# Optimization experiments

Measured on AMD Instinct MI355X. Metric: run time of the kernel, lower is better.

## Reference

```python
import jax, jax.numpy as jnp
import numpy as np

D_MODEL = 1024
NUM_HEADS = 16
DEPTH = D_MODEL // NUM_HEADS
B, S = 2, 2048
NEG = -1e9


def setup_inputs() -> dict:
    key = jax.random.key(0)
    ks = jax.random.split(key, 12)
    sc = 1.0 / np.sqrt(D_MODEL)
    inp = {
        "query": jax.random.normal(ks[0], (B, S, D_MODEL), jnp.float32),
        "key_in": jax.random.normal(ks[1], (B, S, D_MODEL), jnp.float32),
        "value": jax.random.normal(ks[2], (B, S, D_MODEL), jnp.float32),
        # causal mask: 1.0 where attention is disallowed (upper triangle)
        "mask": (1.0 - jnp.tril(jnp.ones((S, S), jnp.float32)))[None, None, :, :],
        "wq": jax.random.normal(ks[3], (D_MODEL, D_MODEL), jnp.float32) * sc,
        "bq": jnp.zeros((D_MODEL,), jnp.float32),
        "wk": jax.random.normal(ks[4], (D_MODEL, D_MODEL), jnp.float32) * sc,
        "bk": jnp.zeros((D_MODEL,), jnp.float32),
        "wv": jax.random.normal(ks[5], (D_MODEL, D_MODEL), jnp.float32) * sc,
        "bv": jnp.zeros((D_MODEL,), jnp.float32),
        "wo": jax.random.normal(ks[6], (D_MODEL, D_MODEL), jnp.float32) * sc,
        "bo": jnp.zeros((D_MODEL,), jnp.float32),
    }
    return inp


def _split_heads(x):
    # [B,S,D] -> [B,H,S,depth]
    b, s, _ = x.shape
    return x.reshape(b, s, NUM_HEADS, DEPTH).transpose(0, 2, 1, 3)


def reference(query, key_in, value, mask, wq, bq, wk, bk, wv, bv, wo, bo):
    q = _split_heads(query @ wq + bq)
    k = _split_heads(key_in @ wk + bk)
    v = _split_heads(value @ wv + bv)
    scale = 1.0 / jnp.sqrt(jnp.asarray(DEPTH, jnp.float32))
    logits = jnp.einsum("bhqd,bhkd->bhqk", q, k) * scale + mask * NEG
    attn = jax.nn.softmax(logits, axis=-1)
    out = jnp.einsum("bhqk,bhkd->bhqd", attn, v)  # [B,H,S,depth]
    out = out.transpose(0, 2, 1, 3).reshape(query.shape[0], -1, D_MODEL)
    return out @ wo + bo
```

## Files before the change

### kernel.cpp

```cpp
#include <hip/hip_runtime.h>
#include <hip/hip_bf16.h>
#include <cstdint>
#include <cstddef>

#define D_MODEL 1024
#define NHEADS  16
#define DEPTH   64
#define BATCH   2
#define SEQ     2048
#define M_TOT   (BATCH*SEQ)
#define QK_SCALE 0.18033688011112042f

typedef __attribute__((ext_vector_type(8)))  __bf16 bf16x8;
typedef __attribute__((ext_vector_type(4)))  float  f32x4;
typedef __attribute__((ext_vector_type(16))) float  f32x16;

__device__ inline unsigned short f2bf(float f){
  unsigned u = __float_as_uint(f);
  u += 0x7FFFu + ((u>>16)&1u);
  return (unsigned short)(u>>16);
}
__device__ inline unsigned cvtpk(float lo, float hi){
  unsigned r;
  asm("v_cvt_pk_bf16_f32 %0, %1, %2" : "=v"(r) : "v"(lo), "v"(hi));
  return r;
}
__device__ inline float fexp2(float x){
  float r;
  asm("v_exp_f32 %0, %1" : "=v"(r) : "v"(x));
  return r;
}
__device__ inline int bswap23(int x){
  return (x & ~12) | ((x & 4) << 1) | ((x & 8) >> 1);
}

#define AS1(p) ((__attribute__((address_space(1))) void*)(p))
#define AS3(p) ((__attribute__((address_space(3))) void*)(p))

__global__ void cvt3(const float* __restrict__ q, const float* __restrict__ k,
                     const float* __restrict__ v,
                     unsigned short* oq, unsigned short* ok, unsigned short* ov, int n4){
  const float* in = blockIdx.z==0 ? q : blockIdx.z==1 ? k : v;
  unsigned short* out = blockIdx.z==0 ? oq : blockIdx.z==1 ? ok : ov;
  int i = blockIdx.x*blockDim.x + threadIdx.x;
  if (i >= n4) return;
  float4 val = ((const float4*)in)[i];
  ushort4 o;
  o.x = f2bf(val.x); o.y = f2bf(val.y); o.z = f2bf(val.z); o.w = f2bf(val.w);
  ((ushort4*)out)[i] = o;
}

__global__ void tcvt4(const float* __restrict__ w0, const float* __restrict__ w1,
                      const float* __restrict__ w2, const float* __restrict__ w3,
                      unsigned short* o0, unsigned short* o1,
                      unsigned short* o2, unsigned short* o3){
  const float* W = blockIdx.z==0 ? w0 : blockIdx.z==1 ? w1 : blockIdx.z==2 ? w2 : w3;
  unsigned short* Wt = blockIdx.z==0 ? o0 : blockIdx.z==1 ? o1 : blockIdx.z==2 ? o2 : o3;
  const bool perm = (blockIdx.z == 3);
  __shared__ float t[32][33];
  int bx = blockIdx.x*32, by = blockIdx.y*32;
  for (int j = threadIdx.y; j < 32; j += 8)
    t[j][threadIdx.x] = W[(size_t)(by+j)*D_MODEL + bx + threadIdx.x];
  __syncthreads();
  for (int j = threadIdx.y; j < 32; j += 8){
    int col = by + threadIdx.x;
    if (perm) col = bswap23(col);
    Wt[(size_t)(bx+j)*D_MODEL + col] = f2bf(t[threadIdx.x][j]);
  }
}

#define BM 128
#define BN 128
#define BK 32
#define GK 1024

#define GEMM_BODY(As, Bs, Abase, Bbase, acc) \
  for (int k0 = 0; k0 < GK; k0 += BK){ \
    _Pragma("unroll") \
    for (int c=0;c<2;c++){ \
      __builtin_amdgcn_global_load_lds( \
        AS1(Abase + (size_t)(c*64 + (tid>>2))*(GK*2) + k0*2 + (tid&3)*16), \
        AS3((char*)As + c*4096 + tid*16), 16, 0, 0); \
      __builtin_amdgcn_global_load_lds( \
        AS1(Bbase + (size_t)(c*64 + (tid>>2))*(GK*2) + k0*2 + (tid&3)*16), \
        AS3((char*)Bs + c*4096 + tid*16), 16, 0, 0); \
    } \
    __syncthreads(); \
    bf16x8 af[4], bfv[4]; \
    _Pragma("unroll") \
    for (int i=0;i<4;i++) \
      af[i] = *(const bf16x8*)((const char*)As + (wm*64 + i*16 + (lane&15))*64 + (lane>>4)*16); \
    _Pragma("unroll") \
    for (int j=0;j<4;j++) \
      bfv[j] = *(const bf16x8*)((const char*)Bs + (wn*64 + j*16 + (lane&15))*64 + (lane>>4)*16); \
    _Pragma("unroll") \
    for (int i=0;i<4;i++) \
      _Pragma("unroll") \
      for (int j=0;j<4;j++) \
        acc[i][j] = __builtin_amdgcn_mfma_f32_16x16x32_bf16(af[i], bfv[j], acc[i][j], 0,0,0); \
    __syncthreads(); \
  }

__global__ __launch_bounds__(256,2) void gemm_qkv(
    const unsigned short* __restrict__ Xq, const unsigned short* __restrict__ Xk,
    const unsigned short* __restrict__ Xv,
    const unsigned short* __restrict__ Wq, const unsigned short* __restrict__ Wk,
    const unsigned short* __restrict__ Wv,
    const float* __restrict__ bq, const float* __restrict__ bk, const float* __restrict__ bv,
    unsigned short* Qh, unsigned short* Kh, unsigned short* Vth)
{
  __shared__ __align__(16) short As[BM*BK];
  __shared__ __align__(16) short Bs[BN*BK];
  const int z = blockIdx.z;
  const unsigned short* A  = z==0 ? Xq : z==1 ? Xk : Xv;
  const unsigned short* Bt = z==0 ? Wq : z==1 ? Wk : Wv;
  const float* bias        = z==0 ? bq : z==1 ? bk : bv;

  const int tid = threadIdx.x, lane = tid & 63, wave = tid >> 6;
  const int m0 = blockIdx.x*BM, n0 = blockIdx.y*BN;
  const int wm = wave >> 1, wn = wave & 1;

  f32x4 acc[4][4];
  #pragma unroll
  for (int i=0;i<4;i++)
    #pragma unroll
    for (int j=0;j<4;j++)
      acc[i][j] = (f32x4){0.f,0.f,0.f,0.f};

  const char* Abase = (const char*)A + (size_t)m0*GK*2;
  const char* Bbase = (const char*)Bt + (size_t)n0*GK*2;

  GEMM_BODY(As, Bs, Abase, Bbase, acc)

  #pragma unroll
  for (int i=0;i<4;i++)
    #pragma unroll
    for (int j=0;j<4;j++)
      #pragma unroll
      for (int r=0;r<4;r++){
        int gr = m0 + wm*64 + i*16 + (lane>>4)*4 + r;
        int gc = n0 + wn*64 + j*16 + (lane&15);
        float v = acc[i][j][r] + bias[gc];
        int b = gr>>11, s = gr&2047, h = gc>>6, d = gc&63;
        if (z == 0){
          v *= QK_SCALE;
          Qh[(((size_t)(b*NHEADS+h))*SEQ + s)*DEPTH + d] = f2bf(v);
        } else if (z == 1){
          Kh[(((size_t)(b*NHEADS+h))*SEQ + s)*DEPTH + d] = f2bf(v);
        } else {
          int sp = bswap23(s);
          Vth[(((size_t)(b*NHEADS+h))*DEPTH + d)*SEQ + sp] = f2bf(v);
        }
      }
}

#define BM2 64
__global__ __launch_bounds__(256,2) void gemm_out(
    const unsigned short* __restrict__ A,
    const unsigned short* __restrict__ Bt,
    const float* __restrict__ bias,
    float* __restrict__ Cout)
{
  __shared__ __align__(16) short As[BM2*BK];
  __shared__ __align__(16) short Bs[BN*BK];
  const int tid = threadIdx.x, lane = tid & 63, wave = tid >> 6;
  const int m0 = blockIdx.x*BM2, n0 = blockIdx.y*BN;
  const int wm = wave >> 1, wn = wave & 1;

  f32x4 acc[2][4];
  #pragma unroll
  for (int i=0;i<2;i++)
    #pragma unroll
    for (int j=0;j<4;j++)
      acc[i][j] = (f32x4){0.f,0.f,0.f,0.f};

  const char* Abase = (const char*)A + (size_t)m0*GK*2;
  const char* Bbase = (const char*)Bt + (size_t)n0*GK*2;

  for (int k0 = 0; k0 < GK; k0 += BK){
    __builtin_amdgcn_global_load_lds(
      AS1(Abase + (size_t)(tid>>2)*(GK*2) + k0*2 + (tid&3)*16),
      AS3((char*)As + tid*16), 16, 0, 0);
    #pragma unroll
    for (int c=0;c<2;c++)
      __builtin_amdgcn_global_load_lds(
        AS1(Bbase + (size_t)(c*64 + (tid>>2))*(GK*2) + k0*2 + (tid&3)*16),
        AS3((char*)Bs + c*4096 + tid*16), 16, 0, 0);
    __syncthreads();
    bf16x8 af[2], bfv[4];
    #pragma unroll
    for (int i=0;i<2;i++)
      af[i] = *(const bf16x8*)((const char*)As + (wm*32 + i*16 + (lane&15))*64 + (lane>>4)*16);
    #pragma unroll
    for (int j=0;j<4;j++)
      bfv[j] = *(const bf16x8*)((const char*)Bs + (wn*64 + j*16 + (lane&15))*64 + (lane>>4)*16);
    #pragma unroll
    for (int i=0;i<2;i++)
      #pragma unroll
      for (int j=0;j<4;j++)
        acc[i][j] = __builtin_amdgcn_mfma_f32_16x16x32_bf16(af[i], bfv[j], acc[i][j], 0,0,0);
    __syncthreads();
  }

  #pragma unroll
  for (int i=0;i<2;i++)
    #pragma unroll
    for (int j=0;j<4;j++)
      #pragma unroll
      for (int r=0;r<4;r++){
        int gr = m0 + wm*32 + i*16 + (lane>>4)*4 + r;
        int gc = n0 + wn*64 + j*16 + (lane&15);
        Cout[(size_t)gr*D_MODEL + gc] = acc[i][j][r] + bias[gc];
      }
}

__global__ __launch_bounds__(512,4) void attn_fwd(
  const unsigned short* __restrict__ Qh,
  const unsigned short* __restrict__ Kh,
  const unsigned short* __restrict__ Vt,
  unsigned short* __restrict__ AO)
{
  __shared__ __align__(16) short Ks[2][4096];
  __shared__ __align__(16) short Vs[2][4096];
  __shared__ float cbS[2][128];

  const int tid = threadIdx.x, lane = tid & 63, w = tid >> 6;
  const int h = lane >> 5, ql = lane & 31;
  const int qh = w & 1, kh = (w >> 1) & 1, tl = w >> 2;
  const int pj = blockIdx.x, bh = blockIdx.y;
  const size_t hb = (size_t)bh * SEQ * DEPTH;
  const char* Kb = (const char*)(Kh + hb);
  const char* Vb = (const char*)(Vt + hb);
  const unsigned short* Qb = Qh + hb;
  const int bb = bh >> 4, hd = bh & 15;
  const int swz = (ql & 7) << 4;

  auto STAGE = [&](int buf, int t){
    const int kv0 = t*64;
    #pragma unroll
    for (int i=0;i<2;i++){
      int c = (w&3)*2 + i;
      int x = c*1024 + lane*16;
      int row = x >> 7;
      int cb = (x & 127) ^ ((row&7)<<4);
      if (w < 4)
        __builtin_amdgcn_global_load_lds(
          AS1(Kb + (size_t)(kv0+row)*128 + cb),
          AS3((char*)&Ks[buf][0] + c*1024), 16, 0, 0);
      else
        __builtin_amdgcn_global_load_lds(
          AS1(Vb + ((size_t)row*SEQ + kv0)*2 + cb),
          AS3((char*)&Vs[buf][0] + c*1024), 16, 0, 0);
    }
  };

  const int jtw = tl ? pj : (31 - pj);
  const int Q0 = jtw*64 + qh*32;
  const int qmax = Q0 + 31;
  const int Tblock = 32 - pj;

  bf16x8 qreg[4];
  {
    const unsigned short* qp = Qb + (size_t)(Q0 + ql)*DEPTH + h*8;
    #pragma unroll
    for (int c=0;c<4;c++) qreg[c] = *(const bf16x8*)(qp + c*16);
  }

  f32x16 oacc[2];
  #pragma unroll
  for (int dh=0;dh<2;dh++)
    #pragma unroll
    for (int r=0;r<16;r++) oacc[dh][r] = 0.f;
  float s = 0.f;

  STAGE(0, 0);
  __syncthreads();
  int cur = 0;

  #pragma unroll 1
  for (int t = 0; t < Tblock; ++t){
    if (t+1 < Tblock) STAGE(cur^1, t+1);
    const int kvb = t*64 + kh*32;

    if (kvb <= qmax){
      f32x16 sa;
      #pragma unroll
      for (int r=0;r<16;r++) sa[r] = -16.0f;
      #pragma unroll
      for (int c=0;c<4;c++){
        bf16x8 kf = *(const bf16x8*)((const char*)&Ks[cur][0]
                      + (kh*32 + ql)*128 + ((32*c + 16*h) ^ swz));
        sa = __builtin_amdgcn_mfma_f32_32x32x16_bf16(kf, qreg[c], sa, 0,0,0);
      }

      if (kvb + 31 > Q0){
        const int qg = Q0 + ql - kvb;
        #pragma unroll
        for (int r=0;r<16;r++){
          int pos = (r&3) + 8*(r>>2) + 4*h;
          sa[r] = (pos > qg) ? -1e9f : sa[r];
        }
      }

      float s0=0.f, s1=0.f, s2=0.f, s3=0.f;
      #pragma unroll
      for (int r=0;r<16;r++){
        float p = fexp2(sa[r]);
        sa[r] = p;
        if ((r&3)==0) s0 += p; else if ((r&3)==1) s1 += p;
        else if ((r&3)==2) s2 += p; else s3 += p;
      }
      s += (s0+s1)+(s2+s3);

      bf16x8 pw[2];
      #pragma unroll
      for (int ks=0;ks<2;ks++){
        const int mm = 8*ks;
        union { unsigned u[4]; bf16x8 v; } pk;
        pk.u[0] = cvtpk(sa[mm+0], sa[mm+1]);
        pk.u[1] = cvtpk(sa[mm+2], sa[mm+3]);
        pk.u[2] = cvtpk(sa[mm+4], sa[mm+5]);
        pk.u[3] = cvtpk(sa[mm+6], sa[mm+7]);
        pw[ks] = pk.v;
      }

      #pragma unroll
      for (int ks=0;ks<2;ks++){
        #pragma unroll
        for (int dh=0;dh<2;dh++){
          bf16x8 vf = *(const bf16x8*)((const char*)&Vs[cur][0]
                        + (dh*32 + ql)*128 + ((kh*64 + ks*32 + 16*h) ^ swz));
          oacc[dh] = __builtin_amdgcn_mfma_f32_32x32x16_bf16(vf, pw[ks], oacc[dh], 0,0,0);
        }
      }
    }

    __syncthreads();
    cur ^= 1;
  }

  float* cbO  = (tl == 0) ? (float*)&Ks[0][0] : (float*)&Vs[0][0];
  float* cbSp = &cbS[tl][0];
  if (kh == 1){
    #pragma unroll
    for (int dh=0;dh<2;dh++)
      #pragma unroll
      for (int r=0;r<16;r++)
        cbO[(dh*16+r)*128 + qh*64 + lane] = oacc[dh][r];
    cbSp[qh*64 + lane] = s;
  }
  __syncthreads();
  if (kh == 0){
    #pragma unroll
    for (int dh=0;dh<2;dh++)
      #pragma unroll
      for (int r=0;r<16;r++)
        oacc[dh][r] += cbO[(dh*16+r)*128 + qh*64 + lane];
    s += cbSp[qh*64 + lane];
    float st = s + __shfl_xor(s, 32, 64);
    float inv = 1.0f / st;
    #pragma unroll
    for (int dh=0;dh<2;dh++)
      #pragma unroll
      for (int r=0;r<16;r++) oacc[dh][r] *= inv;

    unsigned short* orow = AO + ((size_t)bb*SEQ + (Q0 + ql))*D_MODEL + hd*DEPTH;
    #pragma unroll
    for (int dh=0;dh<2;dh++)
      #pragma unroll
      for (int g=0; g<2; g++){
        uint4 st4;
        st4.x = cvtpk(oacc[dh][8*g+0], oacc[dh][8*g+1]);
        st4.y = cvtpk(oacc[dh][8*g+2], oacc[dh][8*g+3]);
        st4.z = cvtpk(oacc[dh][8*g+4], oacc[dh][8*g+5]);
        st4.w = cvtpk(oacc[dh][8*g+6], oacc[dh][8*g+7]);
        *(uint4*)(orow + dh*32 + g*16 + h*8) = st4;
      }
  }
}

extern "C" void kernel_launch(void* const* d_in, const int* in_sizes, int n_in,
                              void* d_out, int out_size, void* d_ws, size_t ws_size,
                              hipStream_t stream) {
  const float* query  = (const float*)d_in[0];
  const float* key_in = (const float*)d_in[1];
  const float* value  = (const float*)d_in[2];
  const float* wq = (const float*)d_in[4];
  const float* bq = (const float*)d_in[5];
  const float* wk = (const float*)d_in[6];
  const float* bk = (const float*)d_in[7];
  const float* wv = (const float*)d_in[8];
  const float* bv = (const float*)d_in[9];
  const float* wo = (const float*)d_in[10];
  const float* bo = (const float*)d_in[11];

  char* ws = (char*)d_ws;
  const size_t MB = 1u<<20;
  unsigned short* Xq  = (unsigned short*)(ws + 0*MB);
  unsigned short* Xk  = (unsigned short*)(ws + 8*MB);
  unsigned short* Xv  = (unsigned short*)(ws + 16*MB);
  unsigned short* Wtq = (unsigned short*)(ws + 24*MB);
  unsigned short* Wtk = (unsigned short*)(ws + 26*MB);
  unsigned short* Wtv = (unsigned short*)(ws + 28*MB);
  unsigned short* Wto = (unsigned short*)(ws + 30*MB);
  unsigned short* Qh  = (unsigned short*)(ws + 32*MB);
  unsigned short* Kh  = (unsigned short*)(ws + 40*MB);
  unsigned short* Vth = (unsigned short*)(ws + 48*MB);
  unsigned short* AO  = (unsigned short*)(ws + 56*MB);

  const int n4 = (M_TOT*D_MODEL)/4;
  cvt3<<<dim3(n4/256,1,3), 256, 0, stream>>>(query, key_in, value, Xq, Xk, Xv, n4);
  tcvt4<<<dim3(32,32,4), dim3(32,8), 0, stream>>>(wq, wk, wv, wo, Wtq, Wtk, Wtv, Wto);

  gemm_qkv<<<dim3(M_TOT/BM, D_MODEL/BN, 3), 256, 0, stream>>>(
      Xq, Xk, Xv, Wtq, Wtk, Wtv, bq, bk, bv, Qh, Kh, Vth);

  attn_fwd<<<dim3(16, BATCH*NHEADS), 512, 0, stream>>>(Qh, Kh, Vth, AO);

  gemm_out<<<dim3(M_TOT/BM2, D_MODEL/BN), 256, 0, stream>>>(AO, Wto, bo, (float*)d_out);
}
```

Measured before the change: 113.6 us.

## Double GEMM K-tile depth and XOR-swizzle LDS layout to cut bank conflicts

The QKV and output-projection GEMMs now stage a 64-wide K slice per iteration instead of 32, which halves the number of barrier pairs per K loop. The LDS rows become 128 bytes and are XOR-swizzled by row, applied both on the global_load_lds destination mapping and on the fragment reads, to avoid bank conflicts on the MFMA operand loads. The launch-bounds occupancy hint of 2 is removed. LDS use per block roughly doubles, which may reduce how many blocks fit on a CU.

```diff
diff --git a/kernel.cpp b/kernel.cpp
--- a/kernel.cpp
+++ b/kernel.cpp
@@ -71,37 +71,25 @@
 
 #define BM 128
 #define BN 128
-#define BK 32
+#define BK 64
 #define GK 1024
 
-#define GEMM_BODY(As, Bs, Abase, Bbase, acc) \
-  for (int k0 = 0; k0 < GK; k0 += BK){ \
-    _Pragma("unroll") \
-    for (int c=0;c<2;c++){ \
-      __builtin_amdgcn_global_load_lds( \
-        AS1(Abase + (size_t)(c*64 + (tid>>2))*(GK*2) + k0*2 + (tid&3)*16), \
-        AS3((char*)As + c*4096 + tid*16), 16, 0, 0); \
-      __builtin_amdgcn_global_load_lds( \
-        AS1(Bbase + (size_t)(c*64 + (tid>>2))*(GK*2) + k0*2 + (tid&3)*16), \
-        AS3((char*)Bs + c*4096 + tid*16), 16, 0, 0); \
-    } \
-    __syncthreads(); \
-    bf16x8 af[4], bfv[4]; \
-    _Pragma("unroll") \
-    for (int i=0;i<4;i++) \
-      af[i] = *(const bf16x8*)((const char*)As + (wm*64 + i*16 + (lane&15))*64 + (lane>>4)*16); \
-    _Pragma("unroll") \
-    for (int j=0;j<4;j++) \
-      bfv[j] = *(const bf16x8*)((const char*)Bs + (wn*64 + j*16 + (lane&15))*64 + (lane>>4)*16); \
-    _Pragma("unroll") \
-    for (int i=0;i<4;i++) \
-      _Pragma("unroll") \
-      for (int j=0;j<4;j++) \
-        acc[i][j] = __builtin_amdgcn_mfma_f32_16x16x32_bf16(af[i], bfv[j], acc[i][j], 0,0,0); \
-    __syncthreads(); \
-  }
-
-__global__ __launch_bounds__(256,2) void gemm_qkv(
+#define STAGE_TILE(lds, P, RSB, k0, ROWS) \
+  _Pragma("unroll") \
+  for (int i2=0; i2<(ROWS)/32; i2++){ \
+    int x = i2*4096 + tid*16; \
+    int row_ = x >> 7; \
+    int cb_ = (x & 127) ^ ((row_&7)<<4); \
+    __builtin_amdgcn_global_load_lds( \
+      AS1((P) + (size_t)row_*(RSB) + (k0)*2 + cb_), \
+      AS3((char*)(lds) + x), 16, 0, 0); \
+  }
+
+#define FRAG(lds, row_, kk) \
+  (*(const bf16x8*)((const char*)(lds) + (row_)*128 + \
+     (((kk)*64 + (lane>>4)*16) ^ (((row_)&7)<<4))))
+
+__global__ __launch_bounds__(256) void gemm_qkv(
     const unsigned short* __restrict__ Xq, const unsigned short* __restrict__ Xk,
     const unsigned short* __restrict__ Xv,
     const unsigned short* __restrict__ Wq, const unsigned short* __restrict__ Wk,
@@ -130,7 +118,27 @@
   const char* Abase = (const char*)A + (size_t)m0*GK*2;
   const char* Bbase = (const char*)Bt + (size_t)n0*GK*2;
 
-  GEMM_BODY(As, Bs, Abase, Bbase, acc)
+  for (int k0 = 0; k0 < GK; k0 += BK){
+    STAGE_TILE(As, Abase, GK*2, k0, BM)
+    STAGE_TILE(Bs, Bbase, GK*2, k0, BN)
+    __syncthreads();
+    #pragma unroll
+    for (int kk=0;kk<2;kk++){
+      bf16x8 af[4], bfv[4];
+      #pragma unroll
+      for (int i=0;i<4;i++)
+        af[i] = FRAG(As, wm*64 + i*16 + (lane&15), kk);
+      #pragma unroll
+      for (int j=0;j<4;j++)
+        bfv[j] = FRAG(Bs, wn*64 + j*16 + (lane&15), kk);
+      #pragma unroll
+      for (int i=0;i<4;i++)
+        #pragma unroll
+        for (int j=0;j<4;j++)
+          acc[i][j] = __builtin_amdgcn_mfma_f32_16x16x32_bf16(af[i], bfv[j], acc[i][j], 0,0,0);
+    }
+    __syncthreads();
+  }
 
   #pragma unroll
   for (int i=0;i<4;i++)
@@ -155,7 +163,7 @@
 }
 
 #define BM2 64
-__global__ __launch_bounds__(256,2) void gemm_out(
+__global__ __launch_bounds__(256) void gemm_out(
     const unsigned short* __restrict__ A,
     const unsigned short* __restrict__ Bt,
     const float* __restrict__ bias,
@@ -178,27 +186,24 @@
   const char* Bbase = (const char*)Bt + (size_t)n0*GK*2;
 
   for (int k0 = 0; k0 < GK; k0 += BK){
-    __builtin_amdgcn_global_load_lds(
-      AS1(Abase + (size_t)(tid>>2)*(GK*2) + k0*2 + (tid&3)*16),
-      AS3((char*)As + tid*16), 16, 0, 0);
-    #pragma unroll
-    for (int c=0;c<2;c++)
-      __builtin_amdgcn_global_load_lds(
-        AS1(Bbase + (size_t)(c*64 + (tid>>2))*(GK*2) + k0*2 + (tid&3)*16),
-        AS3((char*)Bs + c*4096 + tid*16), 16, 0, 0);
+    STAGE_TILE(As, Abase, GK*2, k0, BM2)
+    STAGE_TILE(Bs, Bbase, GK*2, k0, BN)
     __syncthreads();
-    bf16x8 af[2], bfv[4];
-    #pragma unroll
-    for (int i=0;i<2;i++)
-      af[i] = *(const bf16x8*)((const char*)As + (wm*32 + i*16 + (lane&15))*64 + (lane>>4)*16);
-    #pragma unroll
-    for (int j=0;j<4;j++)
-      bfv[j] = *(const bf16x8*)((const char*)Bs + (wn*64 + j*16 + (lane&15))*64 + (lane>>4)*16);
-    #pragma unroll
-    for (int i=0;i<2;i++)
+    #pragma unroll
+    for (int kk=0;kk<2;kk++){
+      bf16x8 af[2], bfv[4];
+      #pragma unroll
+      for (int i=0;i<2;i++)
+        af[i] = FRAG(As, wm*32 + i*16 + (lane&15), kk);
       #pragma unroll
       for (int j=0;j<4;j++)
-        acc[i][j] = __builtin_amdgcn_mfma_f32_16x16x32_bf16(af[i], bfv[j], acc[i][j], 0,0,0);
+        bfv[j] = FRAG(Bs, wn*64 + j*16 + (lane&15), kk);
+      #pragma unroll
+      for (int i=0;i<2;i++)
+        #pragma unroll
+        for (int j=0;j<4;j++)
+          acc[i][j] = __builtin_amdgcn_mfma_f32_16x16x32_bf16(af[i], bfv[j], acc[i][j], 0,0,0);
+    }
     __syncthreads();
   }
 
```

New measurement: 118.8 us. 4.6% more time.

## Fuse fp32-to-bf16 input conversion into QKV GEMM and double-buffer GEMM loads

Applied to the files above, without the earlier changes.

Drops the separate cvt3 conversion kernel. The QKV GEMM now reads fp32 activations directly into registers, converts them with v_cvt_pk_bf16_f32 and writes them to LDS, while B tiles are double-buffered through direct global-to-LDS loads with custom waitcnt barriers. The output GEMM also double-buffers A and B in LDS so the next tile is loaded while the current one is in MFMA. This removes a full write and re-read of the bf16 activations and one launch, in exchange for more register pressure, twice the fp32 read bandwidth per GEMM tile, and fragile hand-placed vmcnt synchronisation.

```diff
diff --git a/kernel.cpp b/kernel.cpp
--- a/kernel.cpp
+++ b/kernel.cpp
@@ -37,17 +37,15 @@
 #define AS1(p) ((__attribute__((address_space(1))) void*)(p))
 #define AS3(p) ((__attribute__((address_space(3))) void*)(p))
 
-__global__ void cvt3(const float* __restrict__ q, const float* __restrict__ k,
-                     const float* __restrict__ v,
-                     unsigned short* oq, unsigned short* ok, unsigned short* ov, int n4){
-  const float* in = blockIdx.z==0 ? q : blockIdx.z==1 ? k : v;
-  unsigned short* out = blockIdx.z==0 ? oq : blockIdx.z==1 ? ok : ov;
-  int i = blockIdx.x*blockDim.x + threadIdx.x;
-  if (i >= n4) return;
-  float4 val = ((const float4*)in)[i];
-  ushort4 o;
-  o.x = f2bf(val.x); o.y = f2bf(val.y); o.z = f2bf(val.z); o.w = f2bf(val.w);
-  ((ushort4*)out)[i] = o;
+__device__ inline void bar_vm4(){
+  asm volatile("s_waitcnt vmcnt(4)" ::: "memory");
+  __builtin_amdgcn_s_barrier();
+  __builtin_amdgcn_sched_barrier(0);
+}
+__device__ inline void bar_lg(){
+  asm volatile("s_waitcnt lgkmcnt(0)" ::: "memory");
+  __builtin_amdgcn_s_barrier();
+  __builtin_amdgcn_sched_barrier(0);
 }
 
 __global__ void tcvt4(const float* __restrict__ w0, const float* __restrict__ w1,
@@ -74,47 +72,20 @@
 #define BK 32
 #define GK 1024
 
-#define GEMM_BODY(As, Bs, Abase, Bbase, acc) \
-  for (int k0 = 0; k0 < GK; k0 += BK){ \
-    _Pragma("unroll") \
-    for (int c=0;c<2;c++){ \
-      __builtin_amdgcn_global_load_lds( \
-        AS1(Abase + (size_t)(c*64 + (tid>>2))*(GK*2) + k0*2 + (tid&3)*16), \
-        AS3((char*)As + c*4096 + tid*16), 16, 0, 0); \
-      __builtin_amdgcn_global_load_lds( \
-        AS1(Bbase + (size_t)(c*64 + (tid>>2))*(GK*2) + k0*2 + (tid&3)*16), \
-        AS3((char*)Bs + c*4096 + tid*16), 16, 0, 0); \
-    } \
-    __syncthreads(); \
-    bf16x8 af[4], bfv[4]; \
-    _Pragma("unroll") \
-    for (int i=0;i<4;i++) \
-      af[i] = *(const bf16x8*)((const char*)As + (wm*64 + i*16 + (lane&15))*64 + (lane>>4)*16); \
-    _Pragma("unroll") \
-    for (int j=0;j<4;j++) \
-      bfv[j] = *(const bf16x8*)((const char*)Bs + (wn*64 + j*16 + (lane&15))*64 + (lane>>4)*16); \
-    _Pragma("unroll") \
-    for (int i=0;i<4;i++) \
-      _Pragma("unroll") \
-      for (int j=0;j<4;j++) \
-        acc[i][j] = __builtin_amdgcn_mfma_f32_16x16x32_bf16(af[i], bfv[j], acc[i][j], 0,0,0); \
-    __syncthreads(); \
-  }
-
 __global__ __launch_bounds__(256,2) void gemm_qkv(
-    const unsigned short* __restrict__ Xq, const unsigned short* __restrict__ Xk,
-    const unsigned short* __restrict__ Xv,
+    const float* __restrict__ Xfq, const float* __restrict__ Xfk,
+    const float* __restrict__ Xfv,
     const unsigned short* __restrict__ Wq, const unsigned short* __restrict__ Wk,
     const unsigned short* __restrict__ Wv,
     const float* __restrict__ bq, const float* __restrict__ bk, const float* __restrict__ bv,
     unsigned short* Qh, unsigned short* Kh, unsigned short* Vth)
 {
   __shared__ __align__(16) short As[BM*BK];
-  __shared__ __align__(16) short Bs[BN*BK];
+  __shared__ __align__(16) short Bs[2][BN*BK];
   const int z = blockIdx.z;
-  const unsigned short* A  = z==0 ? Xq : z==1 ? Xk : Xv;
-  const unsigned short* Bt = z==0 ? Wq : z==1 ? Wk : Wv;
-  const float* bias        = z==0 ? bq : z==1 ? bk : bv;
+  const float* Af          = z==0 ? Xfq : z==1 ? Xfk : Xfv;
+  const unsigned short* Bt = z==0 ? Wq  : z==1 ? Wk  : Wv;
+  const float* bias        = z==0 ? bq  : z==1 ? bk  : bv;
 
   const int tid = threadIdx.x, lane = tid & 63, wave = tid >> 6;
   const int m0 = blockIdx.x*BM, n0 = blockIdx.y*BN;
@@ -127,10 +98,86 @@
     for (int j=0;j<4;j++)
       acc[i][j] = (f32x4){0.f,0.f,0.f,0.f};
 
-  const char* Abase = (const char*)A + (size_t)m0*GK*2;
+  const char* Afb   = (const char*)Af + (size_t)m0*GK*4;
   const char* Bbase = (const char*)Bt + (size_t)n0*GK*2;
-
-  GEMM_BODY(As, Bs, Abase, Bbase, acc)
+  const int arow = tid >> 2;
+  const int acb  = (tid & 3) * 32;
+
+  float4 alo0[2], ahi0[2], alo1[2], ahi1[2];
+
+#define LOADA(LO, HI, k0) \
+  _Pragma("unroll") \
+  for (int c=0;c<2;c++){ \
+    const char* p_ = Afb + (size_t)(c*64 + arow)*(GK*4) + (size_t)(k0)*4 + acb; \
+    LO[c] = *(const float4*)p_; HI[c] = *(const float4*)(p_ + 16); }
+
+#define ISSUEB(t) \
+  _Pragma("unroll") \
+  for (int c=0;c<2;c++) \
+    __builtin_amdgcn_global_load_lds( \
+      AS1(Bbase + (size_t)(c*64 + arow)*(GK*2) + (t)*64 + (tid&3)*16), \
+      AS3((char*)&Bs[(t)&1][0] + c*4096 + tid*16), 16, 0, 0);
+
+#define CVT_WR(LO, HI) { \
+    uint4 pk_[2]; \
+    _Pragma("unroll") \
+    for (int c=0;c<2;c++){ \
+      pk_[c].x = cvtpk(LO[c].x, LO[c].y); pk_[c].y = cvtpk(LO[c].z, LO[c].w); \
+      pk_[c].z = cvtpk(HI[c].x, HI[c].y); pk_[c].w = cvtpk(HI[c].z, HI[c].w); } \
+    bar_vm4(); \
+    _Pragma("unroll") \
+    for (int c=0;c<2;c++) *(uint4*)((char*)As + c*4096 + tid*16) = pk_[c]; \
+    bar_lg(); }
+
+#define CVT_WR_SYNC(LO, HI) { \
+    uint4 pk_[2]; \
+    _Pragma("unroll") \
+    for (int c=0;c<2;c++){ \
+      pk_[c].x = cvtpk(LO[c].x, LO[c].y); pk_[c].y = cvtpk(LO[c].z, LO[c].w); \
+      pk_[c].z = cvtpk(HI[c].x, HI[c].y); pk_[c].w = cvtpk(HI[c].z, HI[c].w); } \
+    __syncthreads(); \
+    _Pragma("unroll") \
+    for (int c=0;c<2;c++) *(uint4*)((char*)As + c*4096 + tid*16) = pk_[c]; \
+    __syncthreads(); }
+
+#define MFMA_PHASE(BUF) { \
+    bf16x8 af_[4], bfv_[4]; \
+    _Pragma("unroll") \
+    for (int i=0;i<4;i++) \
+      af_[i] = *(const bf16x8*)((const char*)As + (wm*64+i*16+(lane&15))*64 + (lane>>4)*16); \
+    _Pragma("unroll") \
+    for (int j=0;j<4;j++) \
+      bfv_[j] = *(const bf16x8*)((const char*)&Bs[BUF][0] + (wn*64+j*16+(lane&15))*64 + (lane>>4)*16); \
+    _Pragma("unroll") \
+    for (int i=0;i<4;i++) \
+      _Pragma("unroll") \
+      for (int j=0;j<4;j++) \
+        acc[i][j] = __builtin_amdgcn_mfma_f32_16x16x32_bf16(af_[i], bfv_[j], acc[i][j], 0,0,0); }
+
+  ISSUEB(0)
+  __builtin_amdgcn_sched_barrier(0);
+  LOADA(alo0, ahi0, 0)
+  LOADA(alo1, ahi1, 32)
+
+  #pragma unroll 1
+  for (int k0 = 0; k0 < 960; k0 += 64){
+    const int t = k0 >> 5;
+    CVT_WR(alo0, ahi0)
+    ISSUEB(t+1)
+    __builtin_amdgcn_sched_barrier(0);
+    LOADA(alo0, ahi0, k0+64)
+    MFMA_PHASE(t&1)
+    CVT_WR(alo1, ahi1)
+    ISSUEB(t+2)
+    __builtin_amdgcn_sched_barrier(0);
+    LOADA(alo1, ahi1, k0+96)
+    MFMA_PHASE((t+1)&1)
+  }
+  CVT_WR_SYNC(alo0, ahi0)
+  ISSUEB(31)
+  MFMA_PHASE(0)
+  CVT_WR_SYNC(alo1, ahi1)
+  MFMA_PHASE(1)
 
   #pragma unroll
   for (int i=0;i<4;i++)
@@ -152,6 +199,11 @@
           Vth[(((size_t)(b*NHEADS+h))*DEPTH + d)*SEQ + sp] = f2bf(v);
         }
       }
+#undef LOADA
+#undef ISSUEB
+#undef CVT_WR
+#undef CVT_WR_SYNC
+#undef MFMA_PHASE
 }
 
 #define BM2 64
@@ -161,8 +213,8 @@
     const float* __restrict__ bias,
     float* __restrict__ Cout)
 {
-  __shared__ __align__(16) short As[BM2*BK];
-  __shared__ __align__(16) short Bs[BN*BK];
+  __shared__ __align__(16) short As[2][BM2*BK];
+  __shared__ __align__(16) short Bs[2][BN*BK];
   const int tid = threadIdx.x, lane = tid & 63, wave = tid >> 6;
   const int m0 = blockIdx.x*BM2, n0 = blockIdx.y*BN;
   const int wm = wave >> 1, wn = wave & 1;
@@ -177,29 +229,34 @@
   const char* Abase = (const char*)A + (size_t)m0*GK*2;
   const char* Bbase = (const char*)Bt + (size_t)n0*GK*2;
 
-  for (int k0 = 0; k0 < GK; k0 += BK){
+  auto STAGE = [&](int t){
     __builtin_amdgcn_global_load_lds(
-      AS1(Abase + (size_t)(tid>>2)*(GK*2) + k0*2 + (tid&3)*16),
-      AS3((char*)As + tid*16), 16, 0, 0);
+      AS1(Abase + (size_t)(tid>>2)*(GK*2) + t*64 + (tid&3)*16),
+      AS3((char*)&As[t&1][0] + tid*16), 16, 0, 0);
     #pragma unroll
     for (int c=0;c<2;c++)
       __builtin_amdgcn_global_load_lds(
-        AS1(Bbase + (size_t)(c*64 + (tid>>2))*(GK*2) + k0*2 + (tid&3)*16),
-        AS3((char*)Bs + c*4096 + tid*16), 16, 0, 0);
+        AS1(Bbase + (size_t)(c*64 + (tid>>2))*(GK*2) + t*64 + (tid&3)*16),
+        AS3((char*)&Bs[t&1][0] + c*4096 + tid*16), 16, 0, 0);
+  };
+
+  STAGE(0);
+  #pragma unroll 1
+  for (int t = 0; t < 32; ++t){
     __syncthreads();
+    if (t+1 < 32) STAGE(t+1);
     bf16x8 af[2], bfv[4];
     #pragma unroll
     for (int i=0;i<2;i++)
-      af[i] = *(const bf16x8*)((const char*)As + (wm*32 + i*16 + (lane&15))*64 + (lane>>4)*16);
+      af[i] = *(const bf16x8*)((const char*)&As[t&1][0] + (wm*32 + i*16 + (lane&15))*64 + (lane>>4)*16);
     #pragma unroll
     for (int j=0;j<4;j++)
-      bfv[j] = *(const bf16x8*)((const char*)Bs + (wn*64 + j*16 + (lane&15))*64 + (lane>>4)*16);
+      bfv[j] = *(const bf16x8*)((const char*)&Bs[t&1][0] + (wn*64 + j*16 + (lane&15))*64 + (lane>>4)*16);
     #pragma unroll
     for (int i=0;i<2;i++)
       #pragma unroll
       for (int j=0;j<4;j++)
         acc[i][j] = __builtin_amdgcn_mfma_f32_16x16x32_bf16(af[i], bfv[j], acc[i][j], 0,0,0);
-    __syncthreads();
   }
 
   #pragma unroll
@@ -396,9 +453,6 @@
 
   char* ws = (char*)d_ws;
   const size_t MB = 1u<<20;
-  unsigned short* Xq  = (unsigned short*)(ws + 0*MB);
-  unsigned short* Xk  = (unsigned short*)(ws + 8*MB);
-  unsigned short* Xv  = (unsigned short*)(ws + 16*MB);
   unsigned short* Wtq = (unsigned short*)(ws + 24*MB);
   unsigned short* Wtk = (unsigned short*)(ws + 26*MB);
   unsigned short* Wtv = (unsigned short*)(ws + 28*MB);
@@ -408,12 +462,10 @@
   unsigned short* Vth = (unsigned short*)(ws + 48*MB);
   unsigned short* AO  = (unsigned short*)(ws + 56*MB);
 
-  const int n4 = (M_TOT*D_MODEL)/4;
-  cvt3<<<dim3(n4/256,1,3), 256, 0, stream>>>(query, key_in, value, Xq, Xk, Xv, n4);
   tcvt4<<<dim3(32,32,4), dim3(32,8), 0, stream>>>(wq, wk, wv, wo, Wtq, Wtk, Wtv, Wto);
 
   gemm_qkv<<<dim3(M_TOT/BM, D_MODEL/BN, 3), 256, 0, stream>>>(
-      Xq, Xk, Xv, Wtq, Wtk, Wtv, bq, bk, bv, Qh, Kh, Vth);
+      query, key_in, value, Wtq, Wtk, Wtv, bq, bk, bv, Qh, Kh, Vth);
 
   attn_fwd<<<dim3(16, BATCH*NHEADS), 512, 0, stream>>>(Qh, Kh, Vth, AO);
 
```

Measured after the change: 107.6 us. 1.06x faster.
